# Optimization experiments

Hardware: AMD Instinct MI355X
Metric: run time of the kernel (lower is better)

Reference implementation:

```python
import jax, jax.numpy as jnp
import numpy as np


def setup_inputs() -> dict:
    key = jax.random.key(0)
    k1, k2 = jax.random.split(key)
    B, L1, L2, D = 8, 2048, 2048, 1024
    features_1 = jax.random.normal(k1, (B, L1, D), dtype=jnp.float32)
    features_2 = jax.random.normal(k2, (B, L2, D), dtype=jnp.float32)
    return {"features_1": features_1, "features_2": features_2}


def reference(features_1, features_2):
    # similarity: [B, L1, L2], no scaling (matches original)
    sim = jnp.einsum("bmd,bnd->bmn", features_1, features_2)
    # both softmaxes in the original are dim=-1 (row softmax over L2)
    attn = jax.nn.softmax(sim, axis=-1)  # [B, L1, L2]
    attended_1 = jnp.einsum("bmn,bnd->bmd", attn, features_2)   # [B, L1, D]
    attended_2 = jnp.einsum("bmn,bmd->bnd", attn, features_1)   # attn^T @ f1 -> [B, L2, D]
    return (attended_1, attended_2)
```

## Files before the change

kernel.cpp:

```cpp
#include <hip/hip_runtime.h>
#include <hip/hip_fp16.h>

#define LDIM 2048
#define DDIM 1024
#define NB 8

typedef __attribute__((ext_vector_type(8))) _Float16 f16x8;
typedef __attribute__((ext_vector_type(4))) float f32x4;
typedef unsigned int u32;

#define MFMA16(a, b, c) __builtin_amdgcn_mfma_f32_16x16x32_f16(a, b, c, 0, 0, 0)

typedef const __attribute__((address_space(1))) u32* gas_t;
typedef __attribute__((address_space(3))) u32* las_t;

__device__ __forceinline__ void gl16(const _Float16* g, _Float16* l) {
  __builtin_amdgcn_global_load_lds((gas_t)g, (las_t)l, 16, 0, 0);
}

template <int KT, int LDA>
__device__ __forceinline__ void gemm_core(const _Float16* __restrict__ Arow0,
                                          const _Float16* __restrict__ Brow0,
                                          _Float16* sA, _Float16* sB,
                                          f32x4 acc[4][4], int tid) {
  const int w = tid >> 6, lane = tid & 63;
  const int wm = w >> 1, wn = w & 1;
  const int l15 = lane & 15, g4 = lane >> 4;

  const int rb = tid >> 3;
  const int csw = (tid & 7) ^ (rb & 7);
  const _Float16* ga = Arow0 + (size_t)rb * LDA + csw * 8;
  const _Float16* gb = Brow0 + (size_t)rb * LDA + csw * 8;
  _Float16* da = sA + (w << 9);
  _Float16* db = sB + (w << 9);

  for (int kt = 0; kt < KT; ++kt) {
    const size_t ko = (size_t)kt * 64;
#pragma unroll
    for (int is = 0; is < 4; ++is) {
      gl16(ga + (size_t)(is * 32) * LDA + ko, da + is * 2048);
      gl16(gb + (size_t)(is * 32) * LDA + ko, db + is * 2048);
    }
    __syncthreads();
#pragma unroll
    for (int ks = 0; ks < 2; ++ks) {
      const int cs2 = (((ks << 2) + g4) ^ (l15 & 7)) << 3;
      f16x8 af[4], bf[4];
#pragma unroll
      for (int mr = 0; mr < 4; ++mr)
        af[mr] = *(const f16x8*)&sA[(wm * 64 + mr * 16 + l15) * 64 + cs2];
#pragma unroll
      for (int nr = 0; nr < 4; ++nr)
        bf[nr] = *(const f16x8*)&sB[(wn * 64 + nr * 16 + l15) * 64 + cs2];
#pragma unroll
      for (int mr = 0; mr < 4; ++mr)
#pragma unroll
        for (int nr = 0; nr < 4; ++nr)
          acc[mr][nr] = MFMA16(af[mr], bf[nr], acc[mr][nr]);
    }
    __syncthreads();
  }
}

__global__ __launch_bounds__(256)
void k_prep(const float* __restrict__ F1, const float* __restrict__ F2,
            _Float16* __restrict__ H1, _Float16* __restrict__ H2,
            _Float16* __restrict__ H1T, _Float16* __restrict__ H2T) {
  __shared__ _Float16 sT[64][72];
  const int bid = blockIdx.x;
  const int inp = bid >> 12;
  const int rem = bid & 4095;
  const int b = rem >> 9, rt = (rem >> 4) & 31, ct = rem & 15;
  const int r0 = rt * 64, c0 = ct * 64;

  const float* F = (inp ? F2 : F1) + (size_t)b * LDIM * DDIM;
  _Float16* H = (inp ? H2 : H1) + (size_t)b * LDIM * DDIM;
  _Float16* HT = (inp ? H2T : H1T) + (size_t)b * DDIM * LDIM;

  const int t = threadIdx.x;
  const int row = t >> 2, seg = (t & 3) * 16;
  {
    const float* src = F + (size_t)(r0 + row) * DDIM + c0 + seg;
    float4 v0 = *(const float4*)(src), v1 = *(const float4*)(src + 4);
    float4 v2 = *(const float4*)(src + 8), v3 = *(const float4*)(src + 12);
    _Float16 h[16];
#pragma unroll
    for (int j = 0; j < 4; ++j) {
      h[j] = (_Float16)((&v0.x)[j]); h[4 + j] = (_Float16)((&v1.x)[j]);
      h[8 + j] = (_Float16)((&v2.x)[j]); h[12 + j] = (_Float16)((&v3.x)[j]);
    }
    _Float16* dst = H + (size_t)(r0 + row) * DDIM + c0 + seg;
#pragma unroll
    for (int j = 0; j < 16; ++j) dst[j] = h[j];
#pragma unroll
    for (int j = 0; j < 16; ++j) sT[seg + j][row] = h[j];
  }
  __syncthreads();
  {
    const int cloc = t >> 2, rseg = (t & 3) * 16;
    _Float16* dst = HT + (size_t)(c0 + cloc) * LDIM + r0 + rseg;
    *(uint4*)dst = *(const uint4*)&sT[cloc][rseg];
    *(uint4*)(dst + 8) = *(const uint4*)&sT[cloc][rseg + 8];
  }
}

__global__ __launch_bounds__(256, 2)
void k_qk(const _Float16* __restrict__ H1, const _Float16* __restrict__ H2,
          _Float16* __restrict__ P, float2* __restrict__ partials) {
  __shared__ _Float16 sA[8192];
  __shared__ _Float16 sB[8192];
  __shared__ float sRedM[128][2];
  __shared__ float sRedS[128][2];
  __shared__ float sM[128];

  const int tid = threadIdx.x;
  const int lane = tid & 63;
  const int w = tid >> 6, wm = w >> 1, wn = w & 1;
  const int l15 = lane & 15, g4 = lane >> 4;

  const int nwg = gridDim.x;
  const int orig = blockIdx.x;
  const int idx = (orig & 7) * (nwg >> 3) + (orig >> 3);
  const int b = idx >> 8;
  const int mt = (idx >> 4) & 15, nt = idx & 15;
  const int m0 = mt << 7, n0 = nt << 7;

  f32x4 acc[4][4];
#pragma unroll
  for (int i = 0; i < 4; ++i)
#pragma unroll
    for (int j = 0; j < 4; ++j) acc[i][j] = (f32x4){0.f, 0.f, 0.f, 0.f};

  gemm_core<16, 1024>(H1 + (size_t)b * LDIM * DDIM + (size_t)m0 * DDIM,
                      H2 + (size_t)b * LDIM * DDIM + (size_t)n0 * DDIM,
                      sA, sB, acc, tid);

#pragma unroll
  for (int mr = 0; mr < 4; ++mr)
#pragma unroll
    for (int r = 0; r < 4; ++r) {
      float v = fmaxf(fmaxf(acc[mr][0][r], acc[mr][1][r]),
                      fmaxf(acc[mr][2][r], acc[mr][3][r]));
#pragma unroll
      for (int off = 1; off < 16; off <<= 1) v = fmaxf(v, __shfl_xor(v, off, 64));
      if (l15 == 0) sRedM[wm * 64 + mr * 16 + g4 * 4 + r][wn] = v;
    }
  __syncthreads();
  if (tid < 128) sM[tid] = fmaxf(sRedM[tid][0], sRedM[tid][1]);
  __syncthreads();

  _Float16* pOut = P + ((size_t)b << 22);
#pragma unroll
  for (int mr = 0; mr < 4; ++mr)
#pragma unroll
    for (int r = 0; r < 4; ++r) {
      const int rloc = wm * 64 + mr * 16 + g4 * 4 + r;
      const float m = sM[rloc];
      float s = 0.f;
#pragma unroll
      for (int nr = 0; nr < 4; ++nr) {
        float p = __expf(acc[mr][nr][r] - m);
        s += p;
        pOut[(size_t)(m0 + rloc) * LDIM + n0 + wn * 64 + nr * 16 + l15] = (_Float16)p;
      }
#pragma unroll
      for (int off = 1; off < 16; off <<= 1) s += __shfl_xor(s, off, 64);
      if (l15 == 0) sRedS[rloc][wn] = s;
    }
  __syncthreads();
  if (tid < 128) {
    const float l = sRedS[tid][0] + sRedS[tid][1];
    partials[((size_t)(b * 16 + nt) << 11) + m0 + tid] = make_float2(sM[tid], l);
  }
}

__global__ void k_merge(const float2* __restrict__ partials, float* __restrict__ factors) {
  const int t = blockIdx.x * 256 + threadIdx.x;
  if (t >= NB * LDIM) return;
  const int b = t >> 11, row = t & 2047;
  float2 p[16];
  float M = -1e30f;
#pragma unroll
  for (int i = 0; i < 16; ++i) {
    p[i] = partials[((size_t)(b * 16 + i) << 11) + row];
    M = fmaxf(M, p[i].x);
  }
  float L = 0.f;
#pragma unroll
  for (int i = 0; i < 16; ++i) L += p[i].y * __expf(p[i].x - M);
  const float inv = 1.0f / L;
#pragma unroll
  for (int i = 0; i < 16; ++i)
    factors[((size_t)(b * 16 + i) << 11) + row] = __expf(p[i].x - M) * inv;
}

__global__ __launch_bounds__(256)
void k_scale_t(_Float16* __restrict__ P, const float* __restrict__ factors,
               _Float16* __restrict__ PT) {
  __shared__ _Float16 sT[64][72];
  const int bid = blockIdx.x;
  const int b = bid >> 10, mt = (bid >> 5) & 31, nt = bid & 31;
  const int m0 = mt * 64, n0 = nt * 64;
  const int nblk = n0 >> 7;

  _Float16* p = P + ((size_t)b << 22);
  _Float16* pt = PT + ((size_t)b << 22);

  const int t = threadIdx.x;
  const int row = t >> 2, seg = (t & 3) * 16;
  {
    const float f = factors[((size_t)(b * 16 + nblk) << 11) + m0 + row];
    const _Float16 hf = (_Float16)f;
    _Float16* src = p + (size_t)(m0 + row) * LDIM + n0 + seg;
    f16x8 h0 = *(const f16x8*)src, h1 = *(const f16x8*)(src + 8);
#pragma unroll
    for (int j = 0; j < 8; ++j) { h0[j] *= hf; h1[j] *= hf; }
    *(f16x8*)src = h0;
    *(f16x8*)(src + 8) = h1;
#pragma unroll
    for (int j = 0; j < 8; ++j) { sT[seg + j][row] = h0[j]; sT[seg + 8 + j][row] = h1[j]; }
  }
  __syncthreads();
  {
    const int nloc = t >> 2, mseg = (t & 3) * 16;
    _Float16* dst = pt + (size_t)(n0 + nloc) * LDIM + m0 + mseg;
    *(uint4*)dst = *(const uint4*)&sT[nloc][mseg];
    *(uint4*)(dst + 8) = *(const uint4*)&sT[nloc][mseg + 8];
  }
}

__global__ __launch_bounds__(256, 2)
void k_gemm(const _Float16* __restrict__ A, const _Float16* __restrict__ B,
            float* __restrict__ C) {
  __shared__ _Float16 sA[8192];
  __shared__ _Float16 sB[8192];

  const int tid = threadIdx.x;
  const int lane = tid & 63;
  const int w = tid >> 6, wm = w >> 1, wn = w & 1;
  const int l15 = lane & 15, g4 = lane >> 4;

  const int nwg = gridDim.x;
  const int orig = blockIdx.x;
  const int idx = (orig & 7) * (nwg >> 3) + (orig >> 3);
  const int b = idx >> 7;
  const int mt = (idx >> 3) & 15, nt = idx & 7;
  const int m0 = mt << 7, d0 = nt << 7;

  f32x4 acc[4][4];
#pragma unroll
  for (int i = 0; i < 4; ++i)
#pragma unroll
    for (int j = 0; j < 4; ++j) acc[i][j] = (f32x4){0.f, 0.f, 0.f, 0.f};

  gemm_core<32, 2048>(A + ((size_t)b << 22) + (size_t)m0 * LDIM,
                      B + ((size_t)b << 21) + (size_t)d0 * LDIM,
                      sA, sB, acc, tid);

  float* outp = C + (size_t)b * LDIM * DDIM;
#pragma unroll
  for (int mr = 0; mr < 4; ++mr)
#pragma unroll
    for (int nr = 0; nr < 4; ++nr)
#pragma unroll
      for (int r = 0; r < 4; ++r)
        outp[(size_t)(m0 + wm * 64 + mr * 16 + g4 * 4 + r) * DDIM +
             d0 + wn * 64 + nr * 16 + l15] = acc[mr][nr][r];
}

extern "C" void kernel_launch(void* const* d_in, const int* in_sizes, int n_in,
                              void* d_out, int out_size, void* d_ws, size_t ws_size,
                              hipStream_t stream) {
  const float* f1 = (const float*)d_in[0];
  const float* f2 = (const float*)d_in[1];
  float* out1 = (float*)d_out;
  float* out2 = out1 + (size_t)NB * LDIM * DDIM;

  char* ws = (char*)d_ws;
  _Float16* H1T = (_Float16*)(ws);
  _Float16* H2T = (_Float16*)(ws + 33554432ull);
  _Float16* P   = (_Float16*)(ws + 67108864ull);
  _Float16* PT  = (_Float16*)(ws + 134217728ull);
  _Float16* H1  = (_Float16*)(ws + 134217728ull);
  _Float16* H2  = (_Float16*)(ws + 167772160ull);
  float2* partials = (float2*)(ws + 201326592ull);
  float* factors   = (float*)(ws + 203423744ull);

  k_prep<<<dim3(8192), dim3(256), 0, stream>>>(f1, f2, H1, H2, H1T, H2T);
  k_qk<<<dim3(2048), dim3(256), 0, stream>>>(H1, H2, P, partials);
  k_merge<<<dim3(64), dim3(256), 0, stream>>>(partials, factors);
  k_scale_t<<<dim3(8192), dim3(256), 0, stream>>>(P, factors, PT);
  k_gemm<<<dim3(1024), dim3(256), 0, stream>>>(P, H2T, out1);
  k_gemm<<<dim3(1024), dim3(256), 0, stream>>>(PT, H1T, out2);
}
```

Before: 283.7 us.

## Use 256x256 tiles with 8 waves and double-buffered phased GEMM pipeline

Replaces the single-buffered 128x128, 4-wave GEMM core with a 256x256 tile, 8-wave kernel. It double-buffers LDS through direct global-to-LDS loads, uses explicit vmcnt waits and barriers per half-K phase, and raises MFMA priority. The goal is to overlap global loads with MFMA work and raise data reuse per tile, cutting the load stalls of the old load-sync-compute loop. The softmax partial bookkeeping moves to 8 column blocks to match. Grid counts drop to 512 and 256 blocks, which may underfill the 256 CUs or lower occupancy given 128KB of LDS per block.

```diff
diff --git a/kernel.cpp b/kernel.cpp
--- a/kernel.cpp
+++ b/kernel.cpp
@@ -18,48 +18,95 @@
   __builtin_amdgcn_global_load_lds((gas_t)g, (las_t)l, 16, 0, 0);
 }
 
-template <int KT, int LDA>
-__device__ __forceinline__ void gemm_core(const _Float16* __restrict__ Arow0,
-                                          const _Float16* __restrict__ Brow0,
-                                          _Float16* sA, _Float16* sB,
-                                          f32x4 acc[4][4], int tid) {
-  const int w = tid >> 6, lane = tid & 63;
-  const int wm = w >> 1, wn = w & 1;
+#define SBAR() __builtin_amdgcn_s_barrier()
+#define VMCNT(n) asm volatile("s_waitcnt vmcnt(" #n ")" ::: "memory")
+#define LGKM0 asm volatile("s_waitcnt lgkmcnt(0)" ::: "memory")
+#define SCHED0 __builtin_amdgcn_sched_barrier(0)
+
+template <int MH, int KS, int BB, class FS, class FW>
+__device__ __forceinline__ void phase(const _Float16* sh, int base_a, int base_b,
+                                      f32x4 (&acc)[2][4][4], FS stg, FW wt) {
+  f16x8 af[4], bf[4];
+#pragma unroll
+  for (int mr = 0; mr < 4; ++mr)
+    af[mr] = *(const f16x8*)&sh[BB * 32768 + KS * 8192 + MH * 2048 + base_a + mr * 512];
+#pragma unroll
+  for (int nr = 0; nr < 4; ++nr)
+    bf[nr] = *(const f16x8*)&sh[BB * 32768 + 16384 + KS * 8192 + base_b + nr * 512];
+  stg();
+  wt();
+  __builtin_amdgcn_s_barrier();
+  LGKM0;
+  SCHED0;
+  __builtin_amdgcn_s_setprio(1);
+#pragma unroll
+  for (int mr = 0; mr < 4; ++mr)
+#pragma unroll
+    for (int nr = 0; nr < 4; ++nr)
+      acc[MH][mr][nr] = MFMA16(af[mr], bf[nr], acc[MH][mr][nr]);
+  __builtin_amdgcn_s_setprio(0);
+  SCHED0;
+  __builtin_amdgcn_s_barrier();
+}
+
+template <int LDA, int NT>
+__device__ __forceinline__ void gemm8(const _Float16* __restrict__ Ab,
+                                      const _Float16* __restrict__ Bb,
+                                      _Float16* sh, f32x4 (&acc)[2][4][4]) {
+  const int tid = threadIdx.x;
+  const int lane = tid & 63, w = tid >> 6;
+  const int wm = w >> 2, wn = w & 3;
   const int l15 = lane & 15, g4 = lane >> 4;
 
-  const int rb = tid >> 3;
-  const int csw = (tid & 7) ^ (rb & 7);
-  const _Float16* ga = Arow0 + (size_t)rb * LDA + csw * 8;
-  const _Float16* gb = Brow0 + (size_t)rb * LDA + csw * 8;
-  _Float16* da = sA + (w << 9);
-  _Float16* db = sB + (w << 9);
-
-  for (int kt = 0; kt < KT; ++kt) {
-    const size_t ko = (size_t)kt * 64;
-#pragma unroll
-    for (int is = 0; is < 4; ++is) {
-      gl16(ga + (size_t)(is * 32) * LDA + ko, da + is * 2048);
-      gl16(gb + (size_t)(is * 32) * LDA + ko, db + is * 2048);
-    }
-    __syncthreads();
-#pragma unroll
-    for (int ks = 0; ks < 2; ++ks) {
-      const int cs2 = (((ks << 2) + g4) ^ (l15 & 7)) << 3;
-      f16x8 af[4], bf[4];
-#pragma unroll
-      for (int mr = 0; mr < 4; ++mr)
-        af[mr] = *(const f16x8*)&sA[(wm * 64 + mr * 16 + l15) * 64 + cs2];
-#pragma unroll
-      for (int nr = 0; nr < 4; ++nr)
-        bf[nr] = *(const f16x8*)&sB[(wn * 64 + nr * 16 + l15) * 64 + cs2];
-#pragma unroll
-      for (int mr = 0; mr < 4; ++mr)
-#pragma unroll
-        for (int nr = 0; nr < 4; ++nr)
-          acc[mr][nr] = MFMA16(af[mr], bf[nr], acc[mr][nr]);
-    }
-    __syncthreads();
-  }
+  const int sw = (l15 >> 1) & 3;
+  const int chk = (g4 ^ sw) << 3;
+  const int base_a = (wm * 128 + l15) * 32 + chk;
+  const int base_b = (wn * 64 + l15) * 32 + chk;
+
+  const int srow = tid >> 2;
+  const int scg = (tid & 3) ^ ((srow >> 1) & 3);
+  const _Float16* gA = Ab + (size_t)srow * LDA + scg * 8;
+  const _Float16* gB = Bb + (size_t)srow * LDA + scg * 8;
+  _Float16* lw = sh + w * 512;
+
+  auto stgA = [&](int kt, int kh, int tb) {
+    const _Float16* g = gA + (size_t)kt * 64 + kh * 32;
+    _Float16* l = lw + tb * 32768 + kh * 8192;
+    gl16(g, l);
+    gl16(g + (size_t)128 * LDA, l + 4096);
+  };
+  auto stgB = [&](int kt, int kh, int tb) {
+    const _Float16* g = gB + (size_t)kt * 64 + kh * 32;
+    _Float16* l = lw + tb * 32768 + 16384 + kh * 8192;
+    gl16(g, l);
+    gl16(g + (size_t)128 * LDA, l + 4096);
+  };
+
+  stgA(0, 0, 0); stgB(0, 0, 0);
+  stgA(0, 1, 0); stgB(0, 1, 0);
+  stgA(1, 0, 1); stgB(1, 0, 1);
+  VMCNT(8);
+  SBAR();
+
+  for (int t = 0; t + 3 < NT; t += 2) {
+    phase<0, 0, 0>(sh, base_a, base_b, acc, [&] { stgA(t + 1, 1, 1); }, [] {});
+    phase<1, 0, 0>(sh, base_a, base_b, acc, [&] { stgB(t + 1, 1, 1); }, [] { VMCNT(8); });
+    phase<0, 1, 0>(sh, base_a, base_b, acc, [&] { stgA(t + 2, 0, 0); }, [] {});
+    phase<1, 1, 0>(sh, base_a, base_b, acc, [&] { stgB(t + 2, 0, 0); }, [] { VMCNT(8); });
+    phase<0, 0, 1>(sh, base_a, base_b, acc, [&] { stgA(t + 2, 1, 0); }, [] {});
+    phase<1, 0, 1>(sh, base_a, base_b, acc, [&] { stgB(t + 2, 1, 0); }, [] { VMCNT(8); });
+    phase<0, 1, 1>(sh, base_a, base_b, acc, [&] { stgA(t + 3, 0, 1); }, [] {});
+    phase<1, 1, 1>(sh, base_a, base_b, acc, [&] { stgB(t + 3, 0, 1); }, [] { VMCNT(8); });
+  }
+  constexpr int T = NT - 2;
+  phase<0, 0, 0>(sh, base_a, base_b, acc, [&] { stgA(T + 1, 1, 1); }, [] {});
+  phase<1, 0, 0>(sh, base_a, base_b, acc, [&] { stgB(T + 1, 1, 1); }, [] { VMCNT(8); });
+  phase<0, 1, 0>(sh, base_a, base_b, acc, [] {}, [] {});
+  phase<1, 1, 0>(sh, base_a, base_b, acc, [] {}, [] { VMCNT(4); });
+  phase<0, 0, 1>(sh, base_a, base_b, acc, [] {}, [] {});
+  phase<1, 0, 1>(sh, base_a, base_b, acc, [] {}, [] { VMCNT(0); });
+  phase<0, 1, 1>(sh, base_a, base_b, acc, [] {}, [] {});
+  phase<1, 1, 1>(sh, base_a, base_b, acc, [] {}, [] {});
 }
 
 __global__ __launch_bounds__(256)
@@ -104,73 +151,81 @@
   }
 }
 
-__global__ __launch_bounds__(256, 2)
+__global__ __launch_bounds__(512, 2)
 void k_qk(const _Float16* __restrict__ H1, const _Float16* __restrict__ H2,
           _Float16* __restrict__ P, float2* __restrict__ partials) {
-  __shared__ _Float16 sA[8192];
-  __shared__ _Float16 sB[8192];
-  __shared__ float sRedM[128][2];
-  __shared__ float sRedS[128][2];
-  __shared__ float sM[128];
-
+  __shared__ _Float16 sh[65536];
   const int tid = threadIdx.x;
-  const int lane = tid & 63;
-  const int w = tid >> 6, wm = w >> 1, wn = w & 1;
+  const int lane = tid & 63, w = tid >> 6;
+  const int wm = w >> 2, wn = w & 3;
   const int l15 = lane & 15, g4 = lane >> 4;
 
   const int nwg = gridDim.x;
   const int orig = blockIdx.x;
   const int idx = (orig & 7) * (nwg >> 3) + (orig >> 3);
-  const int b = idx >> 8;
-  const int mt = (idx >> 4) & 15, nt = idx & 15;
-  const int m0 = mt << 7, n0 = nt << 7;
-
-  f32x4 acc[4][4];
-#pragma unroll
-  for (int i = 0; i < 4; ++i)
-#pragma unroll
-    for (int j = 0; j < 4; ++j) acc[i][j] = (f32x4){0.f, 0.f, 0.f, 0.f};
-
-  gemm_core<16, 1024>(H1 + (size_t)b * LDIM * DDIM + (size_t)m0 * DDIM,
-                      H2 + (size_t)b * LDIM * DDIM + (size_t)n0 * DDIM,
-                      sA, sB, acc, tid);
-
-#pragma unroll
-  for (int mr = 0; mr < 4; ++mr)
-#pragma unroll
-    for (int r = 0; r < 4; ++r) {
-      float v = fmaxf(fmaxf(acc[mr][0][r], acc[mr][1][r]),
-                      fmaxf(acc[mr][2][r], acc[mr][3][r]));
-#pragma unroll
-      for (int off = 1; off < 16; off <<= 1) v = fmaxf(v, __shfl_xor(v, off, 64));
-      if (l15 == 0) sRedM[wm * 64 + mr * 16 + g4 * 4 + r][wn] = v;
-    }
-  __syncthreads();
-  if (tid < 128) sM[tid] = fmaxf(sRedM[tid][0], sRedM[tid][1]);
+  const int b = idx >> 6, mt = (idx >> 3) & 7, ntb = idx & 7;
+  const int m0 = mt << 8, n0 = ntb << 8;
+
+  f32x4 acc[2][4][4];
+#pragma unroll
+  for (int i = 0; i < 2; ++i)
+#pragma unroll
+    for (int j = 0; j < 4; ++j)
+#pragma unroll
+      for (int k = 0; k < 4; ++k) acc[i][j][k] = (f32x4){0.f, 0.f, 0.f, 0.f};
+
+  gemm8<1024, 16>(H1 + (size_t)b * LDIM * DDIM + (size_t)m0 * DDIM,
+                  H2 + (size_t)b * LDIM * DDIM + (size_t)n0 * DDIM, sh, acc);
+
+  float* sred = (float*)sh;
+  float* sredS = sred + 1024;
+  __syncthreads();
+
+#pragma unroll
+  for (int mh = 0; mh < 2; ++mh)
+#pragma unroll
+    for (int mr = 0; mr < 4; ++mr)
+#pragma unroll
+      for (int r = 0; r < 4; ++r) {
+        float v = fmaxf(fmaxf(acc[mh][mr][0][r], acc[mh][mr][1][r]),
+                        fmaxf(acc[mh][mr][2][r], acc[mh][mr][3][r]));
+        v = fmaxf(v, __shfl_xor(v, 1, 64));
+        v = fmaxf(v, __shfl_xor(v, 2, 64));
+        v = fmaxf(v, __shfl_xor(v, 4, 64));
+        v = fmaxf(v, __shfl_xor(v, 8, 64));
+        if (l15 == 0) sred[(wm * 128 + mh * 64 + mr * 16 + g4 * 4 + r) * 4 + wn] = v;
+      }
   __syncthreads();
 
   _Float16* pOut = P + ((size_t)b << 22);
 #pragma unroll
-  for (int mr = 0; mr < 4; ++mr)
-#pragma unroll
-    for (int r = 0; r < 4; ++r) {
-      const int rloc = wm * 64 + mr * 16 + g4 * 4 + r;
-      const float m = sM[rloc];
-      float s = 0.f;
-#pragma unroll
-      for (int nr = 0; nr < 4; ++nr) {
-        float p = __expf(acc[mr][nr][r] - m);
-        s += p;
-        pOut[(size_t)(m0 + rloc) * LDIM + n0 + wn * 64 + nr * 16 + l15] = (_Float16)p;
+  for (int mh = 0; mh < 2; ++mh)
+#pragma unroll
+    for (int mr = 0; mr < 4; ++mr)
+#pragma unroll
+      for (int r = 0; r < 4; ++r) {
+        const int row = wm * 128 + mh * 64 + mr * 16 + g4 * 4 + r;
+        const float m = fmaxf(fmaxf(sred[row * 4], sred[row * 4 + 1]),
+                              fmaxf(sred[row * 4 + 2], sred[row * 4 + 3]));
+        float s = 0.f;
+#pragma unroll
+        for (int nr = 0; nr < 4; ++nr) {
+          float p = __expf(acc[mh][mr][nr][r] - m);
+          s += p;
+          pOut[(size_t)(m0 + row) * LDIM + n0 + wn * 64 + nr * 16 + l15] = (_Float16)p;
+        }
+        s += __shfl_xor(s, 1, 64);
+        s += __shfl_xor(s, 2, 64);
+        s += __shfl_xor(s, 4, 64);
+        s += __shfl_xor(s, 8, 64);
+        if (l15 == 0) sredS[row * 4 + wn] = s;
       }
-#pragma unroll
-      for (int off = 1; off < 16; off <<= 1) s += __shfl_xor(s, off, 64);
-      if (l15 == 0) sRedS[rloc][wn] = s;
-    }
-  __syncthreads();
-  if (tid < 128) {
-    const float l = sRedS[tid][0] + sRedS[tid][1];
-    partials[((size_t)(b * 16 + nt) << 11) + m0 + tid] = make_float2(sM[tid], l);
+  __syncthreads();
+  if (tid < 256) {
+    const float m = fmaxf(fmaxf(sred[tid * 4], sred[tid * 4 + 1]),
+                          fmaxf(sred[tid * 4 + 2], sred[tid * 4 + 3]));
+    const float L = sredS[tid * 4] + sredS[tid * 4 + 1] + sredS[tid * 4 + 2] + sredS[tid * 4 + 3];
+    partials[((size_t)(b * 8 + ntb) << 11) + m0 + tid] = make_float2(m, L);
   }
 }
 
@@ -178,20 +233,20 @@
   const int t = blockIdx.x * 256 + threadIdx.x;
   if (t >= NB * LDIM) return;
   const int b = t >> 11, row = t & 2047;
-  float2 p[16];
+  float2 p[8];
   float M = -1e30f;
 #pragma unroll
-  for (int i = 0; i < 16; ++i) {
-    p[i] = partials[((size_t)(b * 16 + i) << 11) + row];
+  for (int i = 0; i < 8; ++i) {
+    p[i] = partials[((size_t)(b * 8 + i) << 11) + row];
     M = fmaxf(M, p[i].x);
   }
   float L = 0.f;
 #pragma unroll
-  for (int i = 0; i < 16; ++i) L += p[i].y * __expf(p[i].x - M);
+  for (int i = 0; i < 8; ++i) L += p[i].y * __expf(p[i].x - M);
   const float inv = 1.0f / L;
 #pragma unroll
-  for (int i = 0; i < 16; ++i)
-    factors[((size_t)(b * 16 + i) << 11) + row] = __expf(p[i].x - M) * inv;
+  for (int i = 0; i < 8; ++i)
+    factors[((size_t)(b * 8 + i) << 11) + row] = __expf(p[i].x - M) * inv;
 }
 
 __global__ __launch_bounds__(256)
@@ -201,7 +256,7 @@
   const int bid = blockIdx.x;
   const int b = bid >> 10, mt = (bid >> 5) & 31, nt = bid & 31;
   const int m0 = mt * 64, n0 = nt * 64;
-  const int nblk = n0 >> 7;
+  const int nblk = n0 >> 8;
 
   _Float16* p = P + ((size_t)b << 22);
   _Float16* pt = PT + ((size_t)b << 22);
@@ -209,7 +264,7 @@
   const int t = threadIdx.x;
   const int row = t >> 2, seg = (t & 3) * 16;
   {
-    const float f = factors[((size_t)(b * 16 + nblk) << 11) + m0 + row];
+    const float f = factors[((size_t)(b * 8 + nblk) << 11) + m0 + row];
     const _Float16 hf = (_Float16)f;
     _Float16* src = p + (size_t)(m0 + row) * LDIM + n0 + seg;
     f16x8 h0 = *(const f16x8*)src, h1 = *(const f16x8*)(src + 8);
@@ -229,43 +284,43 @@
   }
 }
 
-__global__ __launch_bounds__(256, 2)
+__global__ __launch_bounds__(512, 2)
 void k_gemm(const _Float16* __restrict__ A, const _Float16* __restrict__ B,
             float* __restrict__ C) {
-  __shared__ _Float16 sA[8192];
-  __shared__ _Float16 sB[8192];
-
+  __shared__ _Float16 sh[65536];
   const int tid = threadIdx.x;
-  const int lane = tid & 63;
-  const int w = tid >> 6, wm = w >> 1, wn = w & 1;
+  const int lane = tid & 63, w = tid >> 6;
+  const int wm = w >> 2, wn = w & 3;
   const int l15 = lane & 15, g4 = lane >> 4;
 
   const int nwg = gridDim.x;
   const int orig = blockIdx.x;
   const int idx = (orig & 7) * (nwg >> 3) + (orig >> 3);
-  const int b = idx >> 7;
-  const int mt = (idx >> 3) & 15, nt = idx & 7;
-  const int m0 = mt << 7, d0 = nt << 7;
-
-  f32x4 acc[4][4];
-#pragma unroll
-  for (int i = 0; i < 4; ++i)
-#pragma unroll
-    for (int j = 0; j < 4; ++j) acc[i][j] = (f32x4){0.f, 0.f, 0.f, 0.f};
-
-  gemm_core<32, 2048>(A + ((size_t)b << 22) + (size_t)m0 * LDIM,
-                      B + ((size_t)b << 21) + (size_t)d0 * LDIM,
-                      sA, sB, acc, tid);
+  const int b = idx >> 5, mt = (idx >> 2) & 7, dt = idx & 3;
+  const int m0 = mt << 8, d0 = dt << 8;
+
+  f32x4 acc[2][4][4];
+#pragma unroll
+  for (int i = 0; i < 2; ++i)
+#pragma unroll
+    for (int j = 0; j < 4; ++j)
+#pragma unroll
+      for (int k = 0; k < 4; ++k) acc[i][j][k] = (f32x4){0.f, 0.f, 0.f, 0.f};
+
+  gemm8<2048, 32>(A + ((size_t)b << 22) + (size_t)m0 * LDIM,
+                  B + ((size_t)b << 21) + (size_t)d0 * LDIM, sh, acc);
 
   float* outp = C + (size_t)b * LDIM * DDIM;
 #pragma unroll
-  for (int mr = 0; mr < 4; ++mr)
-#pragma unroll
-    for (int nr = 0; nr < 4; ++nr)
-#pragma unroll
-      for (int r = 0; r < 4; ++r)
-        outp[(size_t)(m0 + wm * 64 + mr * 16 + g4 * 4 + r) * DDIM +
-             d0 + wn * 64 + nr * 16 + l15] = acc[mr][nr][r];
+  for (int mh = 0; mh < 2; ++mh)
+#pragma unroll
+    for (int mr = 0; mr < 4; ++mr)
+#pragma unroll
+      for (int nr = 0; nr < 4; ++nr)
+#pragma unroll
+        for (int r = 0; r < 4; ++r)
+          outp[(size_t)(m0 + wm * 128 + mh * 64 + mr * 16 + g4 * 4 + r) * DDIM +
+               d0 + wn * 64 + nr * 16 + l15] = acc[mh][mr][nr][r];
 }
 
 extern "C" void kernel_launch(void* const* d_in, const int* in_sizes, int n_in,
@@ -287,9 +342,9 @@
   float* factors   = (float*)(ws + 203423744ull);
 
   k_prep<<<dim3(8192), dim3(256), 0, stream>>>(f1, f2, H1, H2, H1T, H2T);
-  k_qk<<<dim3(2048), dim3(256), 0, stream>>>(H1, H2, P, partials);
+  k_qk<<<dim3(512), dim3(512), 0, stream>>>(H1, H2, P, partials);
   k_merge<<<dim3(64), dim3(256), 0, stream>>>(partials, factors);
   k_scale_t<<<dim3(8192), dim3(256), 0, stream>>>(P, factors, PT);
-  k_gemm<<<dim3(1024), dim3(256), 0, stream>>>(P, H2T, out1);
-  k_gemm<<<dim3(1024), dim3(256), 0, stream>>>(PT, H1T, out2);
-}
+  k_gemm<<<dim3(256), dim3(512), 0, stream>>>(P, H2T, out1);
+  k_gemm<<<dim3(256), dim3(512), 0, stream>>>(PT, H1T, out2);
+}
```

After: 293.3 us. +3.4%, slower.

## Fold softmax normalization into GEMM operand scaling and emit P transpose in QK

Applied to the files above, without the earlier changes.

Removes the separate scale-and-transpose pass over the full P matrix. The per-block softmax correction factors are now applied inside the two output GEMMs: on A fragments in registers, plus a final 1/L scale for attended_1. When the workspace is large enough, the QK kernel also writes the transposed P tile straight from shared memory, so it never has to be re-read from global memory. The cost is extra fp16 multiplies in the GEMM inner loop and extra LDS traffic in the QK epilogue. There is also a workspace-size-dependent fallback path.

```diff
diff --git a/kernel.cpp b/kernel.cpp
--- a/kernel.cpp
+++ b/kernel.cpp
@@ -7,22 +7,25 @@
 
 typedef __attribute__((ext_vector_type(8))) _Float16 f16x8;
 typedef __attribute__((ext_vector_type(4))) float f32x4;
-typedef unsigned int u32;
 
 #define MFMA16(a, b, c) __builtin_amdgcn_mfma_f32_16x16x32_f16(a, b, c, 0, 0, 0)
 
-typedef const __attribute__((address_space(1))) u32* gas_t;
-typedef __attribute__((address_space(3))) u32* las_t;
+typedef const __attribute__((address_space(1))) unsigned int* gas_t;
+typedef __attribute__((address_space(3))) unsigned int* las_t;
 
 __device__ __forceinline__ void gl16(const _Float16* g, _Float16* l) {
   __builtin_amdgcn_global_load_lds((gas_t)g, (las_t)l, 16, 0, 0);
 }
 
-template <int KT, int LDA>
+__device__ __forceinline__ f16x8 splat8(_Float16 x) {
+  return (f16x8){x, x, x, x, x, x, x, x};
+}
+
+template <int KT, int LDA, class F>
 __device__ __forceinline__ void gemm_core(const _Float16* __restrict__ Arow0,
                                           const _Float16* __restrict__ Brow0,
                                           _Float16* sA, _Float16* sB,
-                                          f32x4 acc[4][4], int tid) {
+                                          f32x4 (&acc)[4][4], int tid, F scaleA) {
   const int w = tid >> 6, lane = tid & 63;
   const int wm = w >> 1, wn = w & 1;
   const int l15 = lane & 15, g4 = lane >> 4;
@@ -52,6 +55,7 @@
 #pragma unroll
       for (int nr = 0; nr < 4; ++nr)
         bf[nr] = *(const f16x8*)&sB[(wn * 64 + nr * 16 + l15) * 64 + cs2];
+      scaleA(af, kt, ks);
 #pragma unroll
       for (int mr = 0; mr < 4; ++mr)
 #pragma unroll
@@ -83,17 +87,17 @@
     const float* src = F + (size_t)(r0 + row) * DDIM + c0 + seg;
     float4 v0 = *(const float4*)(src), v1 = *(const float4*)(src + 4);
     float4 v2 = *(const float4*)(src + 8), v3 = *(const float4*)(src + 12);
-    _Float16 h[16];
+    f16x8 ha, hb;
 #pragma unroll
     for (int j = 0; j < 4; ++j) {
-      h[j] = (_Float16)((&v0.x)[j]); h[4 + j] = (_Float16)((&v1.x)[j]);
-      h[8 + j] = (_Float16)((&v2.x)[j]); h[12 + j] = (_Float16)((&v3.x)[j]);
+      ha[j] = (_Float16)((&v0.x)[j]); ha[4 + j] = (_Float16)((&v1.x)[j]);
+      hb[j] = (_Float16)((&v2.x)[j]); hb[4 + j] = (_Float16)((&v3.x)[j]);
     }
     _Float16* dst = H + (size_t)(r0 + row) * DDIM + c0 + seg;
-#pragma unroll
-    for (int j = 0; j < 16; ++j) dst[j] = h[j];
-#pragma unroll
-    for (int j = 0; j < 16; ++j) sT[seg + j][row] = h[j];
+    *(f16x8*)dst = ha;
+    *(f16x8*)(dst + 8) = hb;
+#pragma unroll
+    for (int j = 0; j < 8; ++j) { sT[seg + j][row] = ha[j]; sT[seg + 8 + j][row] = hb[j]; }
   }
   __syncthreads();
   {
@@ -104,11 +108,12 @@
   }
 }
 
+template <bool WPT>
 __global__ __launch_bounds__(256, 2)
 void k_qk(const _Float16* __restrict__ H1, const _Float16* __restrict__ H2,
-          _Float16* __restrict__ P, float2* __restrict__ partials) {
-  __shared__ _Float16 sA[8192];
-  __shared__ _Float16 sB[8192];
+          _Float16* __restrict__ P, _Float16* __restrict__ PT,
+          float2* __restrict__ partials) {
+  __shared__ _Float16 sAB[16384];
   __shared__ float sRedM[128][2];
   __shared__ float sRedS[128][2];
   __shared__ float sM[128];
@@ -133,7 +138,7 @@
 
   gemm_core<16, 1024>(H1 + (size_t)b * LDIM * DDIM + (size_t)m0 * DDIM,
                       H2 + (size_t)b * LDIM * DDIM + (size_t)n0 * DDIM,
-                      sA, sB, acc, tid);
+                      sAB, sAB + 8192, acc, tid, [](f16x8*, int, int) {});
 
 #pragma unroll
   for (int mr = 0; mr < 4; ++mr)
@@ -161,7 +166,12 @@
       for (int nr = 0; nr < 4; ++nr) {
         float p = __expf(acc[mr][nr][r] - m);
         s += p;
-        pOut[(size_t)(m0 + rloc) * LDIM + n0 + wn * 64 + nr * 16 + l15] = (_Float16)p;
+        const _Float16 ph = (_Float16)p;
+        pOut[(size_t)(m0 + rloc) * LDIM + n0 + wn * 64 + nr * 16 + l15] = ph;
+        if constexpr (WPT) {
+          const int ncol = wn * 64 + nr * 16 + l15;
+          sAB[ncol * 128 + (rloc ^ ((l15 & 7) << 4))] = ph;
+        }
       }
 #pragma unroll
       for (int off = 1; off < 16; off <<= 1) s += __shfl_xor(s, off, 64);
@@ -172,9 +182,43 @@
     const float l = sRedS[tid][0] + sRedS[tid][1];
     partials[((size_t)(b * 16 + nt) << 11) + m0 + tid] = make_float2(sM[tid], l);
   }
-}
-
-__global__ void k_merge(const float2* __restrict__ partials, float* __restrict__ factors) {
+  if constexpr (WPT) {
+    const int n_ = tid >> 1, mh = tid & 1;
+    const int swz = (n_ & 7) << 4;
+    _Float16* dst = PT + ((size_t)b << 22) + (size_t)(n0 + n_) * LDIM + m0 + mh * 64;
+#pragma unroll
+    for (int o = 0; o < 8; ++o)
+      *(uint4*)(dst + o * 8) = *(const uint4*)&sAB[n_ * 128 + ((mh * 64 + o * 8) ^ swz)];
+  }
+}
+
+__global__ __launch_bounds__(256)
+void k_pt(const _Float16* __restrict__ P, _Float16* __restrict__ PT) {
+  __shared__ _Float16 sT[64][72];
+  const int bid = blockIdx.x;
+  const int b = bid >> 10, mt = (bid >> 5) & 31, nt = bid & 31;
+  const int m0 = mt * 64, n0 = nt * 64;
+  const _Float16* p = P + ((size_t)b << 22);
+  _Float16* pt = PT + ((size_t)b << 22);
+  const int t = threadIdx.x;
+  const int row = t >> 2, seg = (t & 3) * 16;
+  {
+    const _Float16* src = p + (size_t)(m0 + row) * LDIM + n0 + seg;
+    f16x8 h0 = *(const f16x8*)src, h1 = *(const f16x8*)(src + 8);
+#pragma unroll
+    for (int j = 0; j < 8; ++j) { sT[seg + j][row] = h0[j]; sT[seg + 8 + j][row] = h1[j]; }
+  }
+  __syncthreads();
+  {
+    const int nloc = t >> 2, mseg = (t & 3) * 16;
+    _Float16* dst = pt + (size_t)(n0 + nloc) * LDIM + m0 + mseg;
+    *(uint4*)dst = *(const uint4*)&sT[nloc][mseg];
+    *(uint4*)(dst + 8) = *(const uint4*)&sT[nloc][mseg + 8];
+  }
+}
+
+__global__ void k_merge(const float2* __restrict__ partials, float* __restrict__ g16,
+                        _Float16* __restrict__ h16, float* __restrict__ invL) {
   const int t = blockIdx.x * 256 + threadIdx.x;
   if (t >= NB * LDIM) return;
   const int b = t >> 11, row = t & 2047;
@@ -189,51 +233,24 @@
 #pragma unroll
   for (int i = 0; i < 16; ++i) L += p[i].y * __expf(p[i].x - M);
   const float inv = 1.0f / L;
-#pragma unroll
-  for (int i = 0; i < 16; ++i)
-    factors[((size_t)(b * 16 + i) << 11) + row] = __expf(p[i].x - M) * inv;
-}
-
-__global__ __launch_bounds__(256)
-void k_scale_t(_Float16* __restrict__ P, const float* __restrict__ factors,
-               _Float16* __restrict__ PT) {
-  __shared__ _Float16 sT[64][72];
-  const int bid = blockIdx.x;
-  const int b = bid >> 10, mt = (bid >> 5) & 31, nt = bid & 31;
-  const int m0 = mt * 64, n0 = nt * 64;
-  const int nblk = n0 >> 7;
-
-  _Float16* p = P + ((size_t)b << 22);
-  _Float16* pt = PT + ((size_t)b << 22);
-
-  const int t = threadIdx.x;
-  const int row = t >> 2, seg = (t & 3) * 16;
-  {
-    const float f = factors[((size_t)(b * 16 + nblk) << 11) + m0 + row];
-    const _Float16 hf = (_Float16)f;
-    _Float16* src = p + (size_t)(m0 + row) * LDIM + n0 + seg;
-    f16x8 h0 = *(const f16x8*)src, h1 = *(const f16x8*)(src + 8);
-#pragma unroll
-    for (int j = 0; j < 8; ++j) { h0[j] *= hf; h1[j] *= hf; }
-    *(f16x8*)src = h0;
-    *(f16x8*)(src + 8) = h1;
-#pragma unroll
-    for (int j = 0; j < 8; ++j) { sT[seg + j][row] = h0[j]; sT[seg + 8 + j][row] = h1[j]; }
-  }
-  __syncthreads();
-  {
-    const int nloc = t >> 2, mseg = (t & 3) * 16;
-    _Float16* dst = pt + (size_t)(n0 + nloc) * LDIM + m0 + mseg;
-    *(uint4*)dst = *(const uint4*)&sT[nloc][mseg];
-    *(uint4*)(dst + 8) = *(const uint4*)&sT[nloc][mseg + 8];
+  invL[((size_t)b << 11) + row] = inv;
+#pragma unroll
+  for (int i = 0; i < 16; ++i) {
+    const float g = __expf(p[i].x - M);
+    const size_t o = ((size_t)(b * 16 + i) << 11) + row;
+    g16[o] = g;
+    h16[o] = (_Float16)(g * inv);
   }
 }
 
 __global__ __launch_bounds__(256, 2)
-void k_gemm(const _Float16* __restrict__ A, const _Float16* __restrict__ B,
-            float* __restrict__ C) {
+void k_att1(const _Float16* __restrict__ Pu, const _Float16* __restrict__ H2T,
+            const float* __restrict__ g16, const float* __restrict__ invL,
+            float* __restrict__ Out) {
   __shared__ _Float16 sA[8192];
   __shared__ _Float16 sB[8192];
+  __shared__ float sG[16][128];
+  __shared__ float sL[128];
 
   const int tid = threadIdx.x;
   const int lane = tid & 63;
@@ -243,9 +260,16 @@
   const int nwg = gridDim.x;
   const int orig = blockIdx.x;
   const int idx = (orig & 7) * (nwg >> 3) + (orig >> 3);
-  const int b = idx >> 7;
-  const int mt = (idx >> 3) & 15, nt = idx & 7;
-  const int m0 = mt << 7, d0 = nt << 7;
+  const int b = idx >> 7, mt = (idx >> 3) & 15, dt = idx & 7;
+  const int m0 = mt << 7, d0 = dt << 7;
+
+#pragma unroll
+  for (int i = 0; i < 8; ++i) {
+    const int ix = i * 256 + tid;
+    sG[ix >> 7][ix & 127] = g16[((size_t)(b * 16 + (ix >> 7)) << 11) + m0 + (ix & 127)];
+  }
+  if (tid < 128) sL[tid] = invL[((size_t)b << 11) + m0 + tid];
+  __syncthreads();
 
   f32x4 acc[4][4];
 #pragma unroll
@@ -253,11 +277,75 @@
 #pragma unroll
     for (int j = 0; j < 4; ++j) acc[i][j] = (f32x4){0.f, 0.f, 0.f, 0.f};
 
-  gemm_core<32, 2048>(A + ((size_t)b << 22) + (size_t)m0 * LDIM,
-                      B + ((size_t)b << 21) + (size_t)d0 * LDIM,
-                      sA, sB, acc, tid);
-
-  float* outp = C + (size_t)b * LDIM * DDIM;
+  _Float16 gh[4];
+  auto scaleA = [&](f16x8* af, int kt, int ks) {
+    if (ks == 0 && !(kt & 1)) {
+      const int kb = kt >> 1;
+#pragma unroll
+      for (int mr = 0; mr < 4; ++mr)
+        gh[mr] = (_Float16)sG[kb][wm * 64 + mr * 16 + l15];
+    }
+#pragma unroll
+    for (int mr = 0; mr < 4; ++mr) af[mr] *= splat8(gh[mr]);
+  };
+
+  gemm_core<32, 2048>(Pu + ((size_t)b << 22) + (size_t)m0 * LDIM,
+                      H2T + ((size_t)b << 21) + (size_t)d0 * LDIM,
+                      sA, sB, acc, tid, scaleA);
+
+  float* outp = Out + (size_t)b * LDIM * DDIM;
+#pragma unroll
+  for (int mr = 0; mr < 4; ++mr)
+#pragma unroll
+    for (int r = 0; r < 4; ++r) {
+      const float sl = sL[wm * 64 + mr * 16 + g4 * 4 + r];
+#pragma unroll
+      for (int nr = 0; nr < 4; ++nr)
+        outp[(size_t)(m0 + wm * 64 + mr * 16 + g4 * 4 + r) * DDIM +
+             d0 + wn * 64 + nr * 16 + l15] = acc[mr][nr][r] * sl;
+    }
+}
+
+__global__ __launch_bounds__(256, 2)
+void k_att2(const _Float16* __restrict__ PuT, const _Float16* __restrict__ H1T,
+            const _Float16* __restrict__ h16, float* __restrict__ Out) {
+  __shared__ _Float16 sA[8192];
+  __shared__ _Float16 sB[8192];
+  __shared__ _Float16 sH[2048];
+
+  const int tid = threadIdx.x;
+  const int lane = tid & 63;
+  const int w = tid >> 6, wm = w >> 1, wn = w & 1;
+  const int l15 = lane & 15, g4 = lane >> 4;
+
+  const int nwg = gridDim.x;
+  const int orig = blockIdx.x;
+  const int idx = (orig & 7) * (nwg >> 3) + (orig >> 3);
+  const int b = idx >> 7, mt = (idx >> 3) & 15, dt = idx & 7;
+  const int m0 = mt << 7, d0 = dt << 7;
+
+  *(f16x8*)&sH[tid * 8] =
+      *(const f16x8*)&h16[((size_t)(b * 16 + mt) << 11) + tid * 8];
+  __syncthreads();
+
+  f32x4 acc[4][4];
+#pragma unroll
+  for (int i = 0; i < 4; ++i)
+#pragma unroll
+    for (int j = 0; j < 4; ++j) acc[i][j] = (f32x4){0.f, 0.f, 0.f, 0.f};
+
+  auto scaleA = [&](f16x8* af, int kt, int ks) {
+    const int kc = ((ks << 2) + g4) << 3;
+    const f16x8 hv = *(const f16x8*)&sH[kt * 64 + kc];
+#pragma unroll
+    for (int mr = 0; mr < 4; ++mr) af[mr] *= hv;
+  };
+
+  gemm_core<32, 2048>(PuT + ((size_t)b << 22) + (size_t)m0 * LDIM,
+                      H1T + ((size_t)b << 21) + (size_t)d0 * LDIM,
+                      sA, sB, acc, tid, scaleA);
+
+  float* outp = Out + (size_t)b * LDIM * DDIM;
 #pragma unroll
   for (int mr = 0; mr < 4; ++mr)
 #pragma unroll
@@ -276,20 +364,29 @@
   float* out1 = (float*)d_out;
   float* out2 = out1 + (size_t)NB * LDIM * DDIM;
 
+  const size_t MB = 1048576ull;
   char* ws = (char*)d_ws;
   _Float16* H1T = (_Float16*)(ws);
-  _Float16* H2T = (_Float16*)(ws + 33554432ull);
-  _Float16* P   = (_Float16*)(ws + 67108864ull);
-  _Float16* PT  = (_Float16*)(ws + 134217728ull);
-  _Float16* H1  = (_Float16*)(ws + 134217728ull);
-  _Float16* H2  = (_Float16*)(ws + 167772160ull);
-  float2* partials = (float2*)(ws + 201326592ull);
-  float* factors   = (float*)(ws + 203423744ull);
+  _Float16* H2T = (_Float16*)(ws + 32 * MB);
+  _Float16* P   = (_Float16*)(ws + 64 * MB);
+  _Float16* H1  = (_Float16*)(ws + 128 * MB);
+  _Float16* H2  = (_Float16*)(ws + 160 * MB);
+  float2* partials = (float2*)(ws + 192 * MB);
+  float* g16  = (float*)(ws + 194 * MB);
+  _Float16* h16 = (_Float16*)(ws + 195 * MB);
+  float* invL = (float*)(ws + 195 * MB + 524288);
+
+  const bool fastpt = ws_size >= 260 * MB;
+  _Float16* PT = (_Float16*)(fastpt ? ws + 196 * MB : ws + 128 * MB);
 
   k_prep<<<dim3(8192), dim3(256), 0, stream>>>(f1, f2, H1, H2, H1T, H2T);
-  k_qk<<<dim3(2048), dim3(256), 0, stream>>>(H1, H2, P, partials);
-  k_merge<<<dim3(64), dim3(256), 0, stream>>>(partials, factors);
-  k_scale_t<<<dim3(8192), dim3(256), 0, stream>>>(P, factors, PT);
-  k_gemm<<<dim3(1024), dim3(256), 0, stream>>>(P, H2T, out1);
-  k_gemm<<<dim3(1024), dim3(256), 0, stream>>>(PT, H1T, out2);
-}
+  if (fastpt) {
+    k_qk<true><<<dim3(2048), dim3(256), 0, stream>>>(H1, H2, P, PT, partials);
+  } else {
+    k_qk<false><<<dim3(2048), dim3(256), 0, stream>>>(H1, H2, P, PT, partials);
+    k_pt<<<dim3(8192), dim3(256), 0, stream>>>(P, PT);
+  }
+  k_merge<<<dim3(64), dim3(256), 0, stream>>>(partials, g16, h16, invL);
+  k_att1<<<dim3(1024), dim3(256), 0, stream>>>(P, H2T, g16, invL, out1);
+  k_att2<<<dim3(1024), dim3(256), 0, stream>>>(PT, H1T, h16, out2);
+}
```

Measured after the change: 351.2 us. 23.8% more time.
